# Kernel optimization log

Measured on AMD Instinct MI355X. Metric: run time of the kernel, lower is better.

The kernel has to match this reference:

```python
import jax, jax.numpy as jnp
import numpy as np

WS = 8        # window size (square)
HEADS = 8
DIM = 512
EPS = 1e-5


def _ln(x, g, b):
    m = x.mean(-1, keepdims=True)
    v = x.var(-1, keepdims=True)
    return (x - m) / jnp.sqrt(v + EPS) * g + b


def _bn(x, g, b, m, v):
    # eval-mode BatchNorm2d on NCHW
    sh = (1, -1, 1, 1)
    return (x - m.reshape(sh)) / jnp.sqrt(v.reshape(sh) + EPS) * g.reshape(sh) + b.reshape(sh)


def _win_rev(w, H, W, C):
    # (B*nW, WS*WS, C) -> (B, C, H, W)
    x = w.reshape(-1, H // WS, W // WS, WS, WS, C)
    return x.transpose(0, 5, 1, 3, 2, 4).reshape(-1, C, H, W)


def _win_part(x):
    # (B, C, H, W) -> (B*nW, WS*WS, C)
    B, C, H, W = x.shape
    x = x.reshape(B, C, H // WS, WS, W // WS, WS)
    return x.transpose(0, 2, 4, 3, 5, 1).reshape(-1, WS * WS, C)


def setup_inputs() -> dict:
    key = jax.random.key(0)
    ks = iter(jax.random.split(key, 64))
    def nrm(sh, s=0.02):
        return jax.random.normal(next(ks), sh, jnp.float32) * s
    C, C2, C8 = DIM, DIM // 2, DIM // 8
    B, H, W = 2, 224, 224
    N = WS * WS
    B_ = B * (H // WS) * (W // WS)
    # relative position index (same construction as the torch module)
    coords = np.stack(np.meshgrid(np.arange(WS), np.arange(WS), indexing='ij'))
    cf = coords.reshape(2, -1)
    rel = (cf[:, :, None] - cf[:, None, :]).transpose(1, 2, 0).astype(np.int64)
    rel[:, :, 0] += WS - 1
    rel[:, :, 1] += WS - 1
    rel[:, :, 0] *= 2 * WS - 1
    rel_idx = jnp.asarray(rel.sum(-1), jnp.int32)   # (N, N)
    ones = lambda n: jnp.ones((n,), jnp.float32)
    zeros = lambda n: jnp.zeros((n,), jnp.float32)
    return dict(
        x=jax.random.normal(next(ks), (B_, N, C), jnp.float32),
        w_pa=nrm((C, C2)), b_pa=zeros(C2),
        g_lna=ones(C2) + nrm((C2,), 0.1), b_lna=nrm((C2,), 0.1),
        w_pc=nrm((C, C)), b_pc=zeros(C),
        g_lnc=ones(C) + nrm((C,), 0.1), b_lnc=nrm((C,), 0.1),
        dw_w=nrm((C, 1, 3, 3), 0.1), dw_b=zeros(C),
        g_bn1=ones(C), b_bn1=zeros(C), m_bn1=nrm((C,), 0.1), v_bn1=ones(C),
        ci_w1=nrm((C, C8)), ci_b1=zeros(C8),
        g_bn2=ones(C8), b_bn2=zeros(C8), m_bn2=nrm((C8,), 0.1), v_bn2=ones(C8),
        ci_w2=nrm((C8, C2)), ci_b2=zeros(C2),
        pj_w=nrm((C, C2)), pj_b=zeros(C2),
        g_bn3=ones(C2), b_bn3=zeros(C2), m_bn3=nrm((C2,), 0.1), v_bn3=ones(C2),
        w_qkv=nrm((C2, 3 * C2)), b_qkv=zeros(3 * C2),
        si_w1=nrm((C2, C8)), si_b1=zeros(C8),
        g_bn4=ones(C8), b_bn4=zeros(C8), m_bn4=nrm((C8,), 0.1), v_bn4=ones(C8),
        si_w2=nrm((C8, 1)), si_b2=zeros(1),
        g_lno=ones(C2) + nrm((C2,), 0.1), b_lno=nrm((C2,), 0.1),
        w_out=nrm((C, C)), b_out=zeros(C),
        rpb=nrm(((2 * WS - 1) ** 2, HEADS)),
        rel_idx=rel_idx, H=H, W=W,
    )


def _forward(x, w_pa, b_pa, g_lna, b_lna, w_pc, b_pc, g_lnc, b_lnc,
             dw_w, dw_b, g_bn1, b_bn1, m_bn1, v_bn1,
             ci_w1, ci_b1, g_bn2, b_bn2, m_bn2, v_bn2, ci_w2, ci_b2,
             pj_w, pj_b, g_bn3, b_bn3, m_bn3, v_bn3,
             w_qkv, b_qkv,
             si_w1, si_b1, g_bn4, b_bn4, m_bn4, v_bn4, si_w2, si_b2,
             g_lno, b_lno, w_out, b_out, rpb, rel_idx, H, W):
    B_, N, C = x.shape
    C2 = C // 2
    hd = C2 // HEADS
    scale = hd ** -0.5
    x_att = _ln(x @ w_pa + b_pa, g_lna, b_lna)            # (B_, N, C2)
    x_cnn = _ln(x @ w_pc + b_pc, g_lnc, b_lnc)            # (B_, N, C)
    x_cnn = _win_rev(x_cnn, H, W, C)                      # (B, C, H, W)
    # depthwise 3x3 conv + BN + GELU
    x_cnn = jax.lax.conv_general_dilated(
        x_cnn, dw_w, (1, 1), [(1, 1), (1, 1)],
        feature_group_count=C, dimension_numbers=('NCHW', 'OIHW', 'NCHW')
    ) + dw_b.reshape(1, -1, 1, 1)
    x_cnn = jax.nn.gelu(_bn(x_cnn, g_bn1, b_bn1, m_bn1, v_bn1), approximate=False)
    # channel interaction: global avg pool -> 1x1 conv -> BN -> GELU -> 1x1 conv
    ci = x_cnn.mean((2, 3))                               # (B, C)
    ci = ci @ ci_w1 + ci_b1                               # (B, C/8)
    ci = jax.nn.gelu((ci - m_bn2) / jnp.sqrt(v_bn2 + EPS) * g_bn2 + b_bn2, approximate=False)
    ci = ci @ ci_w2 + ci_b2                               # (B, C2)
    x_cnn = jnp.einsum('bchw,co->bohw', x_cnn, pj_w) + pj_b.reshape(1, -1, 1, 1)  # (B, C2, H, W)
    # windowed multi-head attention
    qkv = (x_att @ w_qkv + b_qkv).reshape(B_, N, 3, HEADS, hd).transpose(2, 0, 3, 1, 4)
    q, k, v = qkv[0], qkv[1], qkv[2]                      # (B_, heads, N, hd)
    B = ci.shape[0]
    gate = jax.nn.sigmoid(ci).reshape(B, 1, HEADS, 1, hd)
    v = (v.reshape(B, -1, HEADS, N, hd) * gate).reshape(B_, HEADS, N, hd)
    attn = jnp.einsum('bhnd,bhmd->bhnm', q * scale, k)    # (B_, heads, N, N)
    bias = rpb[rel_idx[:N, :N].reshape(-1)].reshape(N, N, HEADS).transpose(2, 0, 1)
    attn = jax.nn.softmax(attn + bias[None], axis=-1)
    x_att = jnp.einsum('bhnm,bhmd->bnhd', attn, v).reshape(B_, N, C2)
    # spatial interaction gating of the conv branch
    x_sp = _win_rev(x_att, H, W, C2)                      # (B, C2, H, W)
    si = jnp.einsum('bchw,co->bohw', x_sp, si_w1) + si_b1.reshape(1, -1, 1, 1)
    si = jax.nn.gelu(_bn(si, g_bn4, b_bn4, m_bn4, v_bn4), approximate=False)
    si = jnp.einsum('bchw,co->bohw', si, si_w2) + si_b2.reshape(1, -1, 1, 1)      # (B, 1, H, W)
    x_cnn = _bn(jax.nn.sigmoid(si) * x_cnn, g_bn3, b_bn3, m_bn3, v_bn3)
    x_cnn = _win_part(x_cnn)                              # (B_, N, C2)
    x_att = _ln(x_att, g_lno, b_lno)
    return jnp.concatenate([x_att, x_cnn], axis=-1) @ w_out + b_out


def reference(x, w_pa, b_pa, g_lna, b_lna, w_pc, b_pc, g_lnc, b_lnc,
              dw_w, dw_b, g_bn1, b_bn1, m_bn1, v_bn1,
              ci_w1, ci_b1, g_bn2, b_bn2, m_bn2, v_bn2, ci_w2, ci_b2,
              pj_w, pj_b, g_bn3, b_bn3, m_bn3, v_bn3,
              w_qkv, b_qkv,
              si_w1, si_b1, g_bn4, b_bn4, m_bn4, v_bn4, si_w2, si_b2,
              g_lno, b_lno, w_out, b_out, rpb, rel_idx, H, W):
    return _forward(x, w_pa, b_pa, g_lna, b_lna, w_pc, b_pc, g_lnc, b_lnc,
                    dw_w, dw_b, g_bn1, b_bn1, m_bn1, v_bn1,
                    ci_w1, ci_b1, g_bn2, b_bn2, m_bn2, v_bn2, ci_w2, ci_b2,
                    pj_w, pj_b, g_bn3, b_bn3, m_bn3, v_bn3,
                    w_qkv, b_qkv,
                    si_w1, si_b1, g_bn4, b_bn4, m_bn4, v_bn4, si_w2, si_b2,
                    g_lno, b_lno, w_out, b_out, rpb, rel_idx, H, W)
```

## Files before the change

### kernel.cpp

```cpp
#include <hip/hip_runtime.h>
#include <math.h>

#define EPS 1e-5f
#define MROWS 100352
#define NWIN  1568

typedef __attribute__((ext_vector_type(8))) short bf16x8;
typedef __attribute__((ext_vector_type(4))) float f32x4;

__device__ __forceinline__ unsigned short f2bf(float f) {
  unsigned u = __float_as_uint(f);
  u += 0x7fffu + ((u >> 16) & 1u);
  return (unsigned short)(u >> 16);
}
__device__ __forceinline__ float bf2f(unsigned short s) {
  return __uint_as_float(((unsigned)s) << 16);
}
__device__ __forceinline__ float gelu_exact(float x) {
  return 0.5f * x * (1.f + erff(x * 0.70710678118654752f));
}

#define GLOAD16(gp, lp)                                              \
  __builtin_amdgcn_global_load_lds(                                  \
      (const __attribute__((address_space(1))) void*)(gp),           \
      (__attribute__((address_space(3))) void*)(lp), 16, 0, 0)

__device__ __forceinline__ void stage_half256(
    const unsigned short* __restrict__ base, int r0, int K, int kk,
    unsigned short* lds, int ldsbase, int tid) {
#pragma unroll
  for (int inst = 0; inst < 2; ++inst) {
    int r = inst * 64 + (tid >> 3);
    int cb = ((tid & 7) << 4) ^ ((r & 7) << 4);
    const unsigned short* src = base + (size_t)(r0 + r) * K + kk + (cb >> 1);
    GLOAD16(src, &lds[ldsbase + inst * 4096 + tid * 8]);
  }
}

__device__ __forceinline__ bf16x8 frag_read256(const unsigned short* lds,
                                               int tilebase, int r_t, int cbyte) {
  int off = r_t * 128 + cbyte;
  int phys = off ^ ((r_t & 7) << 4);
  return *(const bf16x8*)&lds[tilebase + (phys >> 1)];
}

template <bool OUTBF>
__global__ __launch_bounds__(512) void gemm256(
    const unsigned short* __restrict__ A, const unsigned short* __restrict__ Bt,
    const float* __restrict__ bias, void* __restrict__ Cout,
    int M, int N, int K) {
  __shared__ unsigned short lds[65536];
  const int tid = threadIdx.x;
  const int lane = tid & 63, wave = tid >> 6;
  const int wr = wave >> 2, wcn = wave & 3;
  int bx, by;
  {
    const int nwg = gridDim.x * gridDim.y;
    int n = blockIdx.y * gridDim.x + blockIdx.x;
    int w = ((nwg & 7) == 0) ? ((n & 7) * (nwg >> 3) + (n >> 3)) : n;
    by = w / gridDim.x;
    bx = w - by * gridDim.x;
  }
  const int row0 = by * 256, col0 = bx * 256;
  const int rl = lane & 15, qd = lane >> 4;
  f32x4 acc[8][4];
#pragma unroll
  for (int m = 0; m < 8; ++m)
#pragma unroll
    for (int n = 0; n < 4; ++n) acc[m][n] = (f32x4){0.f, 0.f, 0.f, 0.f};

  const int KT = K >> 6;
  stage_half256(A, row0, K, 0, lds, 0, tid);
  stage_half256(A, row0 + 128, K, 0, lds, 8192, tid);
  stage_half256(Bt, col0, K, 0, lds, 16384, tid);
  stage_half256(Bt, col0 + 128, K, 0, lds, 24576, tid);

  for (int kt = 0; kt < KT; ++kt) {
    const int b = kt & 1;
    const int abase = b * 32768, bbase = b * 32768 + 16384;
    const int nb = b ^ 1;
    const int kkn = (kt + 1) << 6;
    const bool last = (kt == KT - 1);
    bf16x8 bfr[4][2];
#pragma unroll
    for (int p = 0; p < 4; ++p) {
      if (!last) {
        if (p == 0)      stage_half256(A, row0, K, kkn, lds, nb * 32768, tid);
        else if (p == 1) stage_half256(A, row0 + 128, K, kkn, lds, nb * 32768 + 8192, tid);
        else if (p == 2) stage_half256(Bt, col0, K, kkn, lds, nb * 32768 + 16384, tid);
        else             stage_half256(Bt, col0 + 128, K, kkn, lds, nb * 32768 + 24576, tid);
      }
      if (p == 0) {
        if (!last) asm volatile("s_waitcnt vmcnt(2)" ::: "memory");
        else       asm volatile("s_waitcnt vmcnt(0)" ::: "memory");
      }
      __builtin_amdgcn_s_barrier();
      __builtin_amdgcn_sched_barrier(0);
      if (p == 0) {
#pragma unroll
        for (int n = 0; n < 4; ++n)
#pragma unroll
          for (int ks = 0; ks < 2; ++ks)
            bfr[n][ks] = frag_read256(lds, bbase, wcn * 64 + n * 16 + rl,
                                      ks * 64 + qd * 16);
      }
      bf16x8 af[2][2];
#pragma unroll
      for (int i = 0; i < 2; ++i)
#pragma unroll
        for (int ks = 0; ks < 2; ++ks)
          af[i][ks] = frag_read256(lds, abase, wr * 128 + (2 * p + i) * 16 + rl,
                                   ks * 64 + qd * 16);
      __builtin_amdgcn_s_setprio(1);
#pragma unroll
      for (int i = 0; i < 2; ++i)
#pragma unroll
        for (int n = 0; n < 4; ++n)
#pragma unroll
          for (int ks = 0; ks < 2; ++ks)
            acc[2 * p + i][n] = __builtin_amdgcn_mfma_f32_16x16x32_bf16(
                af[i][ks], bfr[n][ks], acc[2 * p + i][n], 0, 0, 0);
      __builtin_amdgcn_s_setprio(0);
      __builtin_amdgcn_s_barrier();
    }
  }
  const int crow = qd * 4, ccol = rl;
#pragma unroll
  for (int n = 0; n < 4; ++n) {
    const int gc = col0 + wcn * 64 + n * 16 + ccol;
    const float bz = bias[gc];
#pragma unroll
    for (int m = 0; m < 8; ++m) {
      const int gr0 = row0 + wr * 128 + m * 16 + crow;
#pragma unroll
      for (int r = 0; r < 4; ++r) {
        float val = acc[m][n][r] + bz;
        if constexpr (OUTBF)
          ((unsigned short*)Cout)[(size_t)(gr0 + r) * N + gc] = f2bf(val);
        else
          ((float*)Cout)[(size_t)(gr0 + r) * N + gc] = val;
      }
    }
  }
}

__device__ __forceinline__ void wtc(const float* in, unsigned short* out,
                                    int K, int N, int i) {
  if (i < K * N) {
    int n = i / K, k = i - n * K;
    out[i] = f2bf(in[(size_t)k * N + n]);
  }
}

__global__ __launch_bounds__(256) void prep_all(
    const float* __restrict__ w_pa, const float* __restrict__ w_pc,
    const float* __restrict__ pj_w, const float* __restrict__ w_qkv,
    const float* __restrict__ w_out, const float* __restrict__ si_w1,
    const float* __restrict__ b_pa, const float* __restrict__ b_pc,
    const float* __restrict__ rpb, const int* __restrict__ rel,
    unsigned short* __restrict__ WpaT, unsigned short* __restrict__ WpcT,
    unsigned short* __restrict__ PjT, unsigned short* __restrict__ QkvT,
    unsigned short* __restrict__ OutT, unsigned short* __restrict__ SiT,
    float* __restrict__ B12, float* __restrict__ biasf) {
  const int blk = blockIdx.x, t = threadIdx.x;
  if (blk < 512)        wtc(w_pa, WpaT, 512, 256, blk * 256 + t);
  else if (blk < 1536)  wtc(w_pc, WpcT, 512, 512, (blk - 512) * 256 + t);
  else if (blk < 2048)  wtc(pj_w, PjT, 512, 256, (blk - 1536) * 256 + t);
  else if (blk < 2816)  wtc(w_qkv, QkvT, 256, 768, (blk - 2048) * 256 + t);
  else if (blk < 3840)  wtc(w_out, OutT, 512, 512, (blk - 2816) * 256 + t);
  else if (blk < 3904)  wtc(si_w1, SiT, 256, 64, (blk - 3840) * 256 + t);
  else if (blk == 3904) { B12[t] = b_pa[t]; }
  else if (blk < 3907)  { int i = (blk - 3905) * 256 + t; if (i < 512) B12[256 + i] = b_pc[i]; }
  else {
    int i = (blk - 3907) * 256 + t;
    if (i < 4096) {
      int r = rel[i];
#pragma unroll
      for (int h = 0; h < 8; ++h) biasf[h * 4096 + i] = rpb[r * 8 + h];
    }
  }
}

__global__ __launch_bounds__(256) void cvt_bf16(const float* __restrict__ in,
                                                unsigned short* __restrict__ out,
                                                int n8) {
  int i = blockIdx.x * 256 + threadIdx.x;
  if (i >= n8) return;
  float4 a = ((const float4*)in)[i * 2];
  float4 b = ((const float4*)in)[i * 2 + 1];
  ((ushort4*)out)[i * 2] = make_ushort4(f2bf(a.x), f2bf(a.y), f2bf(a.z), f2bf(a.w));
  ((ushort4*)out)[i * 2 + 1] = make_ushort4(f2bf(b.x), f2bf(b.y), f2bf(b.z), f2bf(b.w));
}

__global__ __launch_bounds__(256) void ln_dual(
    const unsigned short* __restrict__ in,
    unsigned short* __restrict__ outa,
    unsigned short* __restrict__ outc,
    const float* __restrict__ ga, const float* __restrict__ ba,
    const float* __restrict__ gc, const float* __restrict__ bc) {
  const int row = blockIdx.x * 4 + (threadIdx.x >> 6);
  const int t = threadIdx.x & 63;
  const size_t ibase = (size_t)row * 768;
  float va[4], vc[8];
  {
    ushort4 u = *(const ushort4*)&in[ibase + t * 4];
    va[0] = bf2f(u.x); va[1] = bf2f(u.y); va[2] = bf2f(u.z); va[3] = bf2f(u.w);
    ushort4 u0 = *(const ushort4*)&in[ibase + 256 + t * 8];
    ushort4 u1 = *(const ushort4*)&in[ibase + 256 + t * 8 + 4];
    vc[0] = bf2f(u0.x); vc[1] = bf2f(u0.y); vc[2] = bf2f(u0.z); vc[3] = bf2f(u0.w);
    vc[4] = bf2f(u1.x); vc[5] = bf2f(u1.y); vc[6] = bf2f(u1.z); vc[7] = bf2f(u1.w);
  }
  float sa = va[0] + va[1] + va[2] + va[3];
  float qa = va[0]*va[0] + va[1]*va[1] + va[2]*va[2] + va[3]*va[3];
  float sc = 0.f, qc = 0.f;
#pragma unroll
  for (int j = 0; j < 8; ++j) { sc += vc[j]; qc += vc[j] * vc[j]; }
#pragma unroll
  for (int off = 32; off >= 1; off >>= 1) {
    sa += __shfl_xor(sa, off); qa += __shfl_xor(qa, off);
    sc += __shfl_xor(sc, off); qc += __shfl_xor(qc, off);
  }
  const float ma = sa * (1.f / 256.f);
  const float ra = rsqrtf(qa * (1.f / 256.f) - ma * ma + EPS);
  const float mc = sc * (1.f / 512.f);
  const float rc = rsqrtf(qc * (1.f / 512.f) - mc * mc + EPS);
  {
    int c = t * 4;
    *(ushort4*)&outa[(size_t)row * 256 + c] = make_ushort4(
        f2bf((va[0] - ma) * ra * ga[c + 0] + ba[c + 0]),
        f2bf((va[1] - ma) * ra * ga[c + 1] + ba[c + 1]),
        f2bf((va[2] - ma) * ra * ga[c + 2] + ba[c + 2]),
        f2bf((va[3] - ma) * ra * ga[c + 3] + ba[c + 3]));
  }
#pragma unroll
  for (int half = 0; half < 2; ++half) {
    int c = t * 8 + half * 4;
    *(ushort4*)&outc[(size_t)row * 512 + c] = make_ushort4(
        f2bf((vc[half * 4 + 0] - mc) * rc * gc[c + 0] + bc[c + 0]),
        f2bf((vc[half * 4 + 1] - mc) * rc * gc[c + 1] + bc[c + 1]),
        f2bf((vc[half * 4 + 2] - mc) * rc * gc[c + 2] + bc[c + 2]),
        f2bf((vc[half * 4 + 3] - mc) * rc * gc[c + 3] + bc[c + 3]));
  }
}

__global__ __launch_bounds__(256) void dwconv_bn_gelu(
    const unsigned short* __restrict__ xin, const float* __restrict__ wgt9,
    const float* __restrict__ dwb, const float* __restrict__ g1,
    const float* __restrict__ b1, const float* __restrict__ m1,
    const float* __restrict__ v1, unsigned short* __restrict__ outp,
    float* __restrict__ ci_part) {
  __shared__ unsigned short tile[100 * 128];
  __shared__ float psum[8 * 128];
  const int b_ = blockIdx.x;
  const int b = b_ / 784, win = b_ % 784;
  const int wi = win / 28, wj = win % 28;
  const int h0 = wi * 8 - 1, w0 = wj * 8 - 1;
  const int tid = threadIdx.x;
  const int c4 = (tid & 31) * 4;
  const int pg = tid >> 5;
  for (int chunk = 0; chunk < 4; ++chunk) {
    const int c0 = chunk * 128;
    __syncthreads();
#pragma unroll
    for (int it = 0; it < 7; ++it) {
      int idx = it * 256 + tid;
      if (idx < 1600) {
        int p = idx >> 4;
        int ch8 = (idx & 15) * 8;
        int ph = h0 + p / 10, pw = w0 + p % 10;
        uint4 val = {0u, 0u, 0u, 0u};
        if (ph >= 0 && ph < 224 && pw >= 0 && pw < 224) {
          int bs = b * 784 + (ph >> 3) * 28 + (pw >> 3);
          int n = ((ph & 7) << 3) | (pw & 7);
          val = *(const uint4*)&xin[(size_t)(bs * 64 + n) * 512 + c0 + ch8];
        }
        *(uint4*)&tile[p * 128 + ch8] = val;
      }
    }
    __syncthreads();
    float wreg[9][4];
    float scale[4], shift[4], bias0[4];
#pragma unroll
    for (int j = 0; j < 4; ++j) {
      int cc = c0 + c4 + j;
#pragma unroll
      for (int k = 0; k < 9; ++k) wreg[k][j] = wgt9[cc * 9 + k];
      scale[j] = g1[cc] * rsqrtf(v1[cc] + EPS);
      shift[j] = b1[cc] - m1[cc] * scale[j];
      bias0[j] = dwb[cc];
    }
    float cs0 = 0.f, cs1 = 0.f, cs2 = 0.f, cs3 = 0.f;
    for (int q = 0; q < 8; ++q) {
      const int qq = pg * 8 + q;
      const int r = qq >> 3, cc_ = qq & 7;
      float a0 = bias0[0], a1 = bias0[1], a2 = bias0[2], a3 = bias0[3];
#pragma unroll
      for (int dr = 0; dr < 3; ++dr)
#pragma unroll
        for (int dc = 0; dc < 3; ++dc) {
          ushort4 u = *(const ushort4*)&tile[((r + dr) * 10 + cc_ + dc) * 128 + c4];
          const int k = dr * 3 + dc;
          a0 += bf2f(u.x) * wreg[k][0];
          a1 += bf2f(u.y) * wreg[k][1];
          a2 += bf2f(u.z) * wreg[k][2];
          a3 += bf2f(u.w) * wreg[k][3];
        }
      float g0 = gelu_exact(a0 * scale[0] + shift[0]);
      float g1v = gelu_exact(a1 * scale[1] + shift[1]);
      float g2v = gelu_exact(a2 * scale[2] + shift[2]);
      float g3v = gelu_exact(a3 * scale[3] + shift[3]);
      cs0 += g0; cs1 += g1v; cs2 += g2v; cs3 += g3v;
      *(ushort4*)&outp[(size_t)(b_ * 64 + qq) * 512 + c0 + c4] =
          make_ushort4(f2bf(g0), f2bf(g1v), f2bf(g2v), f2bf(g3v));
    }
    *(float4*)&psum[pg * 128 + c4] = make_float4(cs0, cs1, cs2, cs3);
    __syncthreads();
    if (tid < 128) {
      float s = 0.f;
#pragma unroll
      for (int g = 0; g < 8; ++g) s += psum[g * 128 + tid];
      ci_part[(size_t)b_ * 512 + c0 + tid] = s;
    }
  }
}

__global__ __launch_bounds__(512) void ci_reduce(const float* __restrict__ ci_part,
                                                 float* __restrict__ ci_mean) {
  const int b = blockIdx.x, c = threadIdx.x;
  float s = 0.f;
  for (int w = 0; w < 784; ++w) s += ci_part[(size_t)(b * 784 + w) * 512 + c];
  ci_mean[b * 512 + c] = s * (1.f / 50176.f);
}

__global__ __launch_bounds__(512) void ci_gate(
    const float* __restrict__ ci_mean, const float* __restrict__ w1,
    const float* __restrict__ bi1, const float* __restrict__ g2,
    const float* __restrict__ b2, const float* __restrict__ m2,
    const float* __restrict__ v2, const float* __restrict__ w2,
    const float* __restrict__ bi2, float* __restrict__ gate) {
  __shared__ float cm[1024];
  __shared__ float c1[128];
  const int t = threadIdx.x;
  cm[t] = ci_mean[t];
  cm[t + 512] = ci_mean[t + 512];
  __syncthreads();
  if (t < 128) {
    int b = t >> 6, j = t & 63;
    float acc = bi1[j];
    for (int c = 0; c < 512; ++c) acc += cm[b * 512 + c] * w1[c * 64 + j];
    float sc = g2[j] * rsqrtf(v2[j] + EPS);
    c1[t] = gelu_exact((acc - m2[j]) * sc + b2[j]);
  }
  __syncthreads();
  {
    int b = t >> 8, o = t & 255;
    float acc = bi2[o];
#pragma unroll
    for (int j = 0; j < 64; ++j) acc += c1[b * 64 + j] * w2[j * 256 + o];
    gate[b * 256 + o] = 1.f / (1.f + expf(-acc));
  }
}

__global__ __launch_bounds__(256) void attn_si(
    const unsigned short* __restrict__ qkv,
    const unsigned short* __restrict__ xpj,
    const float* __restrict__ gate, const float* __restrict__ biasf,
    const unsigned short* __restrict__ siw1t,
    const float* __restrict__ bi1, const float* __restrict__ g4,
    const float* __restrict__ b4v, const float* __restrict__ m4,
    const float* __restrict__ v4, const float* __restrict__ w2,
    const float* __restrict__ bi2,
    const float* __restrict__ g3, const float* __restrict__ b3v,
    const float* __restrict__ m3, const float* __restrict__ v3,
    const float* __restrict__ glno, const float* __restrict__ blno,
    unsigned short* __restrict__ outc) {
  __shared__ unsigned short smem[26112];
  __shared__ float sig[64];
  const int w = blockIdx.x;
  const int b = w / 784;
  const int tid = threadIdx.x, lane = tid & 63, wave = tid >> 6;
  unsigned short* p_lds = smem + wave * (64 * 68 + 32 * 68);
  unsigned short* vT = p_lds + 64 * 68;
  const int l15 = lane & 15, l4 = lane >> 4;
  const float scale = 0.17677669529663687f;
  f32x4 o0[4][2], o1[4][2];
#pragma unroll
  for (int hh = 0; hh < 2; ++hh) {
    const int h = wave * 2 + hh;
    {
      const float* gh = &gate[b * 256 + h * 32];
      const size_t vbase = ((size_t)w * 64 + lane) * 768 + 512 + h * 32;
#pragma unroll
      for (int c = 0; c < 4; ++c) {
        uint4 vv = *(const uint4*)&qkv[vbase + c * 8];
        float4 gA = *(const float4*)&gh[c * 8];
        float4 gB = *(const float4*)&gh[c * 8 + 4];
        unsigned vw[4] = {vv.x, vv.y, vv.z, vv.w};
        float gg[8] = {gA.x, gA.y, gA.z, gA.w, gB.x, gB.y, gB.z, gB.w};
#pragma unroll
        for (int j = 0; j < 4; ++j) {
          int d = c * 8 + j * 2;
          vT[(d + 0) * 68 + lane] = f2bf(__uint_as_float(vw[j] << 16) * gg[j * 2]);
          vT[(d + 1) * 68 + lane] =
              f2bf(__uint_as_float(vw[j] & 0xffff0000u) * gg[j * 2 + 1]);
        }
      }
    }
    bf16x8 kf[4], qf[4];
    const size_t qkbase = (size_t)w * 64 * 768 + h * 32 + l4 * 8;
#pragma unroll
    for (int t = 0; t < 4; ++t) {
      kf[t] = *(const bf16x8*)&qkv[qkbase + (size_t)(t * 16 + l15) * 768 + 256];
      qf[t] = *(const bf16x8*)&qkv[qkbase + (size_t)(t * 16 + l15) * 768];
    }
    f32x4 s[4][4];
#pragma unroll
    for (int mt = 0; mt < 4; ++mt)
#pragma unroll
      for (int nt = 0; nt < 4; ++nt) s[mt][nt] = (f32x4){0.f, 0.f, 0.f, 0.f};
#pragma unroll
    for (int mt = 0; mt < 4; ++mt)
#pragma unroll
      for (int nt = 0; nt < 4; ++nt)
        s[mt][nt] = __builtin_amdgcn_mfma_f32_16x16x32_bf16(kf[mt], qf[nt],
                                                            s[mt][nt], 0, 0, 0);
    float inv_s[4];
#pragma unroll
    for (int nt = 0; nt < 4; ++nt) {
      float mx = -1e30f;
#pragma unroll
      for (int mt = 0; mt < 4; ++mt) {
        float4 b4 = *(const float4*)&biasf[(h * 64 + nt * 16 + l15) * 64 +
                                           mt * 16 + l4 * 4];
        s[mt][nt][0] = s[mt][nt][0] * scale + b4.x;
        s[mt][nt][1] = s[mt][nt][1] * scale + b4.y;
        s[mt][nt][2] = s[mt][nt][2] * scale + b4.z;
        s[mt][nt][3] = s[mt][nt][3] * scale + b4.w;
#pragma unroll
        for (int r = 0; r < 4; ++r) mx = fmaxf(mx, s[mt][nt][r]);
      }
      mx = fmaxf(mx, __shfl_xor(mx, 16));
      mx = fmaxf(mx, __shfl_xor(mx, 32));
      float sum = 0.f;
#pragma unroll
      for (int mt = 0; mt < 4; ++mt)
#pragma unroll
        for (int r = 0; r < 4; ++r) {
          float e = __expf(s[mt][nt][r] - mx);
          s[mt][nt][r] = e;
          sum += e;
        }
      sum += __shfl_xor(sum, 16);
      sum += __shfl_xor(sum, 32);
      inv_s[nt] = 1.f / sum;
    }
#pragma unroll
    for (int nt = 0; nt < 4; ++nt)
#pragma unroll
      for (int mt = 0; mt < 4; ++mt) {
        ushort4 pk = make_ushort4(f2bf(s[mt][nt][0] * inv_s[nt]),
                                  f2bf(s[mt][nt][1] * inv_s[nt]),
                                  f2bf(s[mt][nt][2] * inv_s[nt]),
                                  f2bf(s[mt][nt][3] * inv_s[nt]));
        *(ushort4*)&p_lds[(nt * 16 + l15) * 68 + mt * 16 + l4 * 4] = pk;
      }
#pragma unroll
    for (int i = 0; i < 4; ++i)
#pragma unroll
      for (int dt = 0; dt < 2; ++dt)
        (hh ? o1 : o0)[i][dt] = (f32x4){0.f, 0.f, 0.f, 0.f};
#pragma unroll
    for (int ks = 0; ks < 2; ++ks) {
      bf16x8 pa[4], vf[2];
#pragma unroll
      for (int i = 0; i < 4; ++i) {
        const unsigned short* pp = &p_lds[(i * 16 + l15) * 68 + ks * 32 + l4 * 8];
        union { bf16x8 v; ushort4 u[2]; } tmp;
        tmp.u[0] = *(const ushort4*)pp;
        tmp.u[1] = *(const ushort4*)(pp + 4);
        pa[i] = tmp.v;
      }
#pragma unroll
      for (int dt = 0; dt < 2; ++dt) {
        const unsigned short* vp = &vT[(dt * 16 + l15) * 68 + ks * 32 + l4 * 8];
        union { bf16x8 v; ushort4 u[2]; } tmp;
        tmp.u[0] = *(const ushort4*)vp;
        tmp.u[1] = *(const ushort4*)(vp + 4);
        vf[dt] = tmp.v;
      }
#pragma unroll
      for (int i = 0; i < 4; ++i)
#pragma unroll
        for (int dt = 0; dt < 2; ++dt)
          (hh ? o1 : o0)[i][dt] = __builtin_amdgcn_mfma_f32_16x16x32_bf16(
              pa[i], vf[dt], (hh ? o1 : o0)[i][dt], 0, 0, 0);
    }
  }
  __syncthreads();
  unsigned short* xattO = smem;
#pragma unroll
  for (int hh = 0; hh < 2; ++hh) {
    const int h = wave * 2 + hh;
#pragma unroll
    for (int i = 0; i < 4; ++i)
#pragma unroll
      for (int dt = 0; dt < 2; ++dt)
#pragma unroll
        for (int r = 0; r < 4; ++r)
          xattO[(i * 16 + l4 * 4 + r) * 264 + h * 32 + dt * 16 + l15] =
              f2bf((hh ? o1 : o0)[i][dt][r]);
  }
  __syncthreads();
  float* s1s = (float*)(smem + 16896);
  {
    f32x4 a4[4];
#pragma unroll
    for (int n = 0; n < 4; ++n) a4[n] = (f32x4){0.f, 0.f, 0.f, 0.f};
#pragma unroll
    for (int ks = 0; ks < 8; ++ks) {
      bf16x8 af = *(const bf16x8*)&xattO[(wave * 16 + l15) * 264 + ks * 32 + l4 * 8];
#pragma unroll
      for (int n = 0; n < 4; ++n) {
        bf16x8 bfr = *(const bf16x8*)&siw1t[(n * 16 + l15) * 256 + ks * 32 + l4 * 8];
        a4[n] = __builtin_amdgcn_mfma_f32_16x16x32_bf16(af, bfr, a4[n], 0, 0, 0);
      }
    }
#pragma unroll
    for (int n = 0; n < 4; ++n) {
      const int j = n * 16 + l15;
      const float sc4 = g4[j] * rsqrtf(v4[j] + EPS);
      const float m4j = m4[j], b4j = b4v[j], bij = bi1[j];
#pragma unroll
      for (int r = 0; r < 4; ++r) {
        float val = (a4[n][r] + bij - m4j) * sc4 + b4j;
        s1s[(wave * 16 + l4 * 4 + r) * 68 + j] = gelu_exact(val);
      }
    }
  }
  __syncthreads();
  if (tid < 64) {
    float a2 = bi2[0];
#pragma unroll
    for (int jj = 0; jj < 64; ++jj) a2 += s1s[tid * 68 + jj] * w2[jj];
    sig[tid] = 1.f / (1.f + expf(-a2));
  }
  __syncthreads();
  {
    const int p = tid >> 2, l = tid & 3;
    float s = 0.f, sq = 0.f;
#pragma unroll
    for (int k = 0; k < 16; ++k) {
      ushort4 u = *(const ushort4*)&xattO[p * 264 + l * 4 + k * 16];
      float x0 = bf2f(u.x), x1 = bf2f(u.y), x2 = bf2f(u.z), x3 = bf2f(u.w);
      s += x0 + x1 + x2 + x3;
      sq += x0 * x0 + x1 * x1 + x2 * x2 + x3 * x3;
    }
    s += __shfl_xor(s, 1);  sq += __shfl_xor(sq, 1);
    s += __shfl_xor(s, 2);  sq += __shfl_xor(sq, 2);
    const float mean = s * (1.f / 256.f);
    const float var = sq * (1.f / 256.f) - mean * mean;
    const float rstd = rsqrtf(var + EPS);
    const size_t orow = ((size_t)w * 64 + p) * 512;
    const float sg = sig[p];
#pragma unroll
    for (int k = 0; k < 16; ++k) {
      const int c = l * 4 + k * 16;
      ushort4 u = *(const ushort4*)&xattO[p * 264 + c];
      *(ushort4*)&outc[orow + c] = make_ushort4(
          f2bf((bf2f(u.x) - mean) * rstd * glno[c + 0] + blno[c + 0]),
          f2bf((bf2f(u.y) - mean) * rstd * glno[c + 1] + blno[c + 1]),
          f2bf((bf2f(u.z) - mean) * rstd * glno[c + 2] + blno[c + 2]),
          f2bf((bf2f(u.w) - mean) * rstd * glno[c + 3] + blno[c + 3]));
      ushort4 pu = *(const ushort4*)&xpj[((size_t)w * 64 + p) * 256 + c];
      float sc0 = g3[c + 0] * rsqrtf(v3[c + 0] + EPS);
      float sc1 = g3[c + 1] * rsqrtf(v3[c + 1] + EPS);
      float sc2 = g3[c + 2] * rsqrtf(v3[c + 2] + EPS);
      float sc3 = g3[c + 3] * rsqrtf(v3[c + 3] + EPS);
      *(ushort4*)&outc[orow + 256 + c] = make_ushort4(
          f2bf(sg * bf2f(pu.x) * sc0 + (b3v[c + 0] - m3[c + 0] * sc0)),
          f2bf(sg * bf2f(pu.y) * sc1 + (b3v[c + 1] - m3[c + 1] * sc1)),
          f2bf(sg * bf2f(pu.z) * sc2 + (b3v[c + 2] - m3[c + 2] * sc2)),
          f2bf(sg * bf2f(pu.w) * sc3 + (b3v[c + 3] - m3[c + 3] * sc3)));
    }
  }
}

extern "C" void kernel_launch(void* const* d_in, const int* in_sizes, int n_in,
                              void* d_out, int out_size, void* d_ws, size_t ws_size,
                              hipStream_t stream) {
  const float* x     = (const float*)d_in[0];
  const float* w_pa  = (const float*)d_in[1];
  const float* b_pa  = (const float*)d_in[2];
  const float* g_lna = (const float*)d_in[3];
  const float* b_lna = (const float*)d_in[4];
  const float* w_pc  = (const float*)d_in[5];
  const float* b_pc  = (const float*)d_in[6];
  const float* g_lnc = (const float*)d_in[7];
  const float* b_lnc = (const float*)d_in[8];
  const float* dw_w  = (const float*)d_in[9];
  const float* dw_b  = (const float*)d_in[10];
  const float* g_bn1 = (const float*)d_in[11];
  const float* b_bn1 = (const float*)d_in[12];
  const float* m_bn1 = (const float*)d_in[13];
  const float* v_bn1 = (const float*)d_in[14];
  const float* ci_w1 = (const float*)d_in[15];
  const float* ci_b1 = (const float*)d_in[16];
  const float* g_bn2 = (const float*)d_in[17];
  const float* b_bn2 = (const float*)d_in[18];
  const float* m_bn2 = (const float*)d_in[19];
  const float* v_bn2 = (const float*)d_in[20];
  const float* ci_w2 = (const float*)d_in[21];
  const float* ci_b2 = (const float*)d_in[22];
  const float* pj_w  = (const float*)d_in[23];
  const float* pj_b  = (const float*)d_in[24];
  const float* g_bn3 = (const float*)d_in[25];
  const float* b_bn3 = (const float*)d_in[26];
  const float* m_bn3 = (const float*)d_in[27];
  const float* v_bn3 = (const float*)d_in[28];
  const float* w_qkv = (const float*)d_in[29];
  const float* b_qkv = (const float*)d_in[30];
  const float* si_w1 = (const float*)d_in[31];
  const float* si_b1 = (const float*)d_in[32];
  const float* g_bn4 = (const float*)d_in[33];
  const float* b_bn4 = (const float*)d_in[34];
  const float* m_bn4 = (const float*)d_in[35];
  const float* v_bn4 = (const float*)d_in[36];
  const float* si_w2 = (const float*)d_in[37];
  const float* si_b2 = (const float*)d_in[38];
  const float* g_lno = (const float*)d_in[39];
  const float* b_lno = (const float*)d_in[40];
  const float* w_out = (const float*)d_in[41];
  const float* b_out = (const float*)d_in[42];
  const float* rpb   = (const float*)d_in[43];
  const int*   rel   = (const int*)d_in[44];

  char* ws = (char*)d_ws;
  unsigned short* G12BF = (unsigned short*)(ws + 0);
  unsigned short* QKVBF = (unsigned short*)(ws + 0);
  unsigned short* A1BF  = (unsigned short*)(ws + 154140672ull);
  unsigned short* C1BF  = (unsigned short*)(ws + 205520896ull);
  unsigned short* CAT   = (unsigned short*)(ws + 205520896ull);
  unsigned short* XBF   = (unsigned short*)(ws + 308281344ull);
  unsigned short* CVBF  = (unsigned short*)(ws + 308281344ull);
  unsigned short* PJBF  = (unsigned short*)(ws + 411041792ull);
  float*          CIP   = (float*)(ws + 462422016ull);
  float*          CIM   = (float*)(ws + 465633280ull);
  float*          GATE  = (float*)(ws + 465637376ull);
  float*          B12   = (float*)(ws + 465639424ull);
  float*          BIASF = (float*)(ws + 465642496ull);
  unsigned short* WT    = (unsigned short*)(ws + 465773568ull);
  unsigned short* WpaT  = WT + 0;
  unsigned short* WpcT  = WT + 131072;
  unsigned short* PjT   = WT + 393216;
  unsigned short* QkvT  = WT + 524288;
  unsigned short* OutT  = WT + 720896;
  unsigned short* SiT   = WT + 983040;

  const int M = MROWS;
  dim3 b256(256), b512(512);

  prep_all<<<3923, b256, 0, stream>>>(w_pa, w_pc, pj_w, w_qkv, w_out, si_w1,
                                      b_pa, b_pc, rpb, rel,
                                      WpaT, WpcT, PjT, QkvT, OutT, SiT,
                                      B12, BIASF);
  cvt_bf16<<<(M * 512 / 8 + 255) / 256, b256, 0, stream>>>(x, XBF, M * 512 / 8);

  gemm256<true><<<dim3(3, M / 256), dim3(512), 0, stream>>>(XBF, WpaT, B12, G12BF,
                                                            M, 768, 512);
  ln_dual<<<M / 4, b256, 0, stream>>>(G12BF, A1BF, C1BF, g_lna, b_lna, g_lnc, b_lnc);

  dwconv_bn_gelu<<<NWIN, b256, 0, stream>>>(C1BF, dw_w, dw_b, g_bn1, b_bn1, m_bn1,
                                            v_bn1, CVBF, CIP);
  ci_reduce<<<2, b512, 0, stream>>>(CIP, CIM);
  ci_gate<<<1, b512, 0, stream>>>(CIM, ci_w1, ci_b1, g_bn2, b_bn2, m_bn2, v_bn2,
                                  ci_w2, ci_b2, GATE);

  gemm256<true><<<dim3(1, M / 256), dim3(512), 0, stream>>>(CVBF, PjT, pj_b, PJBF,
                                                            M, 256, 512);

  gemm256<true><<<dim3(3, M / 256), dim3(512), 0, stream>>>(A1BF, QkvT, b_qkv, QKVBF,
                                                            M, 768, 256);

  attn_si<<<NWIN, b256, 0, stream>>>(QKVBF, PJBF, GATE, BIASF, SiT,
                                     si_b1, g_bn4, b_bn4, m_bn4, v_bn4,
                                     si_w2, si_b2,
                                     g_bn3, b_bn3, m_bn3, v_bn3,
                                     g_lno, b_lno, CAT);

  gemm256<false><<<dim3(2, M / 256), dim3(512), 0, stream>>>(CAT, OutT, b_out,
                                                             (float*)d_out, M, 512, 512);
}
```

Baseline: 816.4 us.

## Shrink attention LDS footprint and fuse spatial-gate reduction via shuffles

```diff
diff --git a/kernel.cpp b/kernel.cpp
--- a/kernel.cpp
+++ b/kernel.cpp
@@ -194,8 +194,7 @@
 
 __global__ __launch_bounds__(256) void ln_dual(
     const unsigned short* __restrict__ in,
-    unsigned short* __restrict__ outa,
-    unsigned short* __restrict__ outc,
+    unsigned short* __restrict__ outa, unsigned short* __restrict__ outc,
     const float* __restrict__ ga, const float* __restrict__ ba,
     const float* __restrict__ gc, const float* __restrict__ bc) {
   const int row = blockIdx.x * 4 + (threadIdx.x >> 6);
@@ -374,13 +373,13 @@
     const float* __restrict__ m3, const float* __restrict__ v3,
     const float* __restrict__ glno, const float* __restrict__ blno,
     unsigned short* __restrict__ outc) {
-  __shared__ unsigned short smem[26112];
+  __shared__ unsigned short smem[17920];
   __shared__ float sig[64];
   const int w = blockIdx.x;
   const int b = w / 784;
   const int tid = threadIdx.x, lane = tid & 63, wave = tid >> 6;
-  unsigned short* p_lds = smem + wave * (64 * 68 + 32 * 68);
-  unsigned short* vT = p_lds + 64 * 68;
+  unsigned short* vT = smem + wave * 4480;
+  unsigned short* ph = vT + 2176;
   const int l15 = lane & 15, l4 = lane >> 4;
   const float scale = 0.17677669529663687f;
   f32x4 o0[4][2], o1[4][2];
@@ -455,26 +454,27 @@
       inv_s[nt] = 1.f / sum;
     }
 #pragma unroll
-    for (int nt = 0; nt < 4; ++nt)
-#pragma unroll
-      for (int mt = 0; mt < 4; ++mt) {
-        ushort4 pk = make_ushort4(f2bf(s[mt][nt][0] * inv_s[nt]),
-                                  f2bf(s[mt][nt][1] * inv_s[nt]),
-                                  f2bf(s[mt][nt][2] * inv_s[nt]),
-                                  f2bf(s[mt][nt][3] * inv_s[nt]));
-        *(ushort4*)&p_lds[(nt * 16 + l15) * 68 + mt * 16 + l4 * 4] = pk;
-      }
-#pragma unroll
     for (int i = 0; i < 4; ++i)
 #pragma unroll
       for (int dt = 0; dt < 2; ++dt)
         (hh ? o1 : o0)[i][dt] = (f32x4){0.f, 0.f, 0.f, 0.f};
 #pragma unroll
     for (int ks = 0; ks < 2; ++ks) {
+#pragma unroll
+      for (int nt = 0; nt < 4; ++nt)
+#pragma unroll
+        for (int mh = 0; mh < 2; ++mh) {
+          const int mt = 2 * ks + mh;
+          ushort4 pk = make_ushort4(f2bf(s[mt][nt][0] * inv_s[nt]),
+                                    f2bf(s[mt][nt][1] * inv_s[nt]),
+                                    f2bf(s[mt][nt][2] * inv_s[nt]),
+                                    f2bf(s[mt][nt][3] * inv_s[nt]));
+          *(ushort4*)&ph[(nt * 16 + l15) * 36 + mh * 16 + l4 * 4] = pk;
+        }
       bf16x8 pa[4], vf[2];
 #pragma unroll
       for (int i = 0; i < 4; ++i) {
-        const unsigned short* pp = &p_lds[(i * 16 + l15) * 68 + ks * 32 + l4 * 8];
+        const unsigned short* pp = &ph[(i * 16 + l15) * 36 + l4 * 8];
         union { bf16x8 v; ushort4 u[2]; } tmp;
         tmp.u[0] = *(const ushort4*)pp;
         tmp.u[1] = *(const ushort4*)(pp + 4);
@@ -511,7 +511,6 @@
               f2bf((hh ? o1 : o0)[i][dt][r]);
   }
   __syncthreads();
-  float* s1s = (float*)(smem + 16896);
   {
     f32x4 a4[4];
 #pragma unroll
@@ -525,24 +524,29 @@
         a4[n] = __builtin_amdgcn_mfma_f32_16x16x32_bf16(af, bfr, a4[n], 0, 0, 0);
       }
     }
+    float part[4] = {0.f, 0.f, 0.f, 0.f};
 #pragma unroll
     for (int n = 0; n < 4; ++n) {
       const int j = n * 16 + l15;
       const float sc4 = g4[j] * rsqrtf(v4[j] + EPS);
-      const float m4j = m4[j], b4j = b4v[j], bij = bi1[j];
-#pragma unroll
-      for (int r = 0; r < 4; ++r) {
-        float val = (a4[n][r] + bij - m4j) * sc4 + b4j;
-        s1s[(wave * 16 + l4 * 4 + r) * 68 + j] = gelu_exact(val);
-      }
-    }
-  }
-  __syncthreads();
-  if (tid < 64) {
-    float a2 = bi2[0];
-#pragma unroll
-    for (int jj = 0; jj < 64; ++jj) a2 += s1s[tid * 68 + jj] * w2[jj];
-    sig[tid] = 1.f / (1.f + expf(-a2));
+      const float m4j = m4[j], b4j = b4v[j], bij = bi1[j], w2j = w2[j];
+#pragma unroll
+      for (int r = 0; r < 4; ++r)
+        part[r] += gelu_exact((a4[n][r] + bij - m4j) * sc4 + b4j) * w2j;
+    }
+#pragma unroll
+    for (int r = 0; r < 4; ++r) {
+      part[r] += __shfl_xor(part[r], 1);
+      part[r] += __shfl_xor(part[r], 2);
+      part[r] += __shfl_xor(part[r], 4);
+      part[r] += __shfl_xor(part[r], 8);
+    }
+    if (l15 == 0) {
+      const float b2v = bi2[0];
+#pragma unroll
+      for (int r = 0; r < 4; ++r)
+        sig[wave * 16 + l4 * 4 + r] = 1.f / (1.f + expf(-(part[r] + b2v)));
+    }
   }
   __syncthreads();
   {
```

New measurement: 817.4 us (median of 2 runs). About the same (+0.1%).
